# Kernel tuning notes

Measured on AMD Instinct MI355X. Metric: run time of the kernel, lower is better.

## Reference

```python
import jax, jax.numpy as jnp
import numpy as np
import math

N_HEADS = 16
D_EMB = 1024
D_HEAD = D_EMB // N_HEADS


def setup_inputs() -> dict:
    key = jax.random.key(0)
    ks = jax.random.split(key, 5)
    scale_in = 1.0 / math.sqrt(D_EMB)
    x = jax.random.normal(ks[0], (2, 2048, D_EMB), dtype=jnp.float32)
    w_in = jax.random.uniform(ks[1], (3 * D_EMB, D_EMB), dtype=jnp.float32, minval=-scale_in, maxval=scale_in)
    b_in = jax.random.uniform(ks[2], (3 * D_EMB,), dtype=jnp.float32, minval=-scale_in, maxval=scale_in)
    w_out = jax.random.uniform(ks[3], (D_EMB, D_EMB), dtype=jnp.float32, minval=-scale_in, maxval=scale_in)
    b_out = jax.random.uniform(ks[4], (D_EMB,), dtype=jnp.float32, minval=-scale_in, maxval=scale_in)
    return {"x": x, "w_in": w_in, "b_in": b_in, "w_out": w_out, "b_out": b_out, "apply_mask": 1}


def reference(x, w_in, b_in, w_out, b_out, apply_mask):
    B, S, D = x.shape
    # fused QKV projection: torch Linear uses y = x @ W^T + b
    qkv = jnp.einsum('bsd,ed->bse', x, w_in) + b_in  # [B,S,3D]
    q, k, v = jnp.split(qkv, 3, axis=-1)
    # [B,H,S,Dh]
    q = q.reshape(B, S, N_HEADS, D_HEAD).transpose(0, 2, 1, 3)
    k = k.reshape(B, S, N_HEADS, D_HEAD).transpose(0, 2, 1, 3)
    v = v.reshape(B, S, N_HEADS, D_HEAD).transpose(0, 2, 1, 3)
    w = jnp.einsum('bhqd,bhkd->bhqk', q, k)  # [B,H,S,S]
    if apply_mask:
        causal = jnp.triu(jnp.ones((S, S), dtype=bool), k=1)
        w = jnp.where(causal, -jnp.inf, w)
    w = w / jnp.sqrt(jnp.float32(D_HEAD)).astype(w.dtype)
    w = jax.nn.softmax(w, axis=-1)
    score = jnp.einsum('bhqk,bhkd->bhqd', w, v)  # [B,H,S,Dh]
    score = score.transpose(0, 2, 1, 3).reshape(B, S, D)
    return jnp.einsum('bsd,ed->bse', score, w_out) + b_out
```

## Files before the change

### kernel.cpp

```cpp
#include <hip/hip_runtime.h>
#include <stdint.h>

#define DEMB 1024
#define NHEAD 16
#define DHEAD 64
#define SEQ 2048
#define MROWS 4096

typedef __bf16 bf16x8 __attribute__((ext_vector_type(8)));
typedef float f32x4 __attribute__((ext_vector_type(4)));
typedef unsigned short u16;

#define LOG2E 1.44269504088896340736f

__device__ __forceinline__ u16 f2b(float f) {
  return __builtin_bit_cast(u16, (__bf16)f);
}
__device__ __forceinline__ uint32_t pk2(float a, float b) {
  return (uint32_t)f2b(a) | ((uint32_t)f2b(b) << 16);
}

__device__ __forceinline__ f32x4 mfma16(bf16x8 a, bf16x8 b, f32x4 c) {
  return __builtin_amdgcn_mfma_f32_16x16x32_bf16(a, b, c, 0, 0, 0);
}

__device__ __forceinline__ void gload_lds16(const void* g, void* l) {
  __builtin_amdgcn_global_load_lds(
      (__attribute__((address_space(1))) unsigned int*)(g),
      (__attribute__((address_space(3))) unsigned int*)(l), 16, 0, 0);
}

__device__ __forceinline__ void tile_barrier() {
  __builtin_amdgcn_sched_barrier(0);
  asm volatile("s_waitcnt vmcnt(0) lgkmcnt(0)" ::: "memory");
  __builtin_amdgcn_s_barrier();
  __builtin_amdgcn_sched_barrier(0);
}

__global__ void cvt3_f32_bf16(const float* __restrict__ a, int na,
                              const float* __restrict__ b, int nb,
                              const float* __restrict__ c, int nc,
                              u16* __restrict__ da, u16* __restrict__ db,
                              u16* __restrict__ dc) {
  const int total = (na + nb + nc) >> 2;
  const int stride = gridDim.x * blockDim.x;
  for (int t = blockIdx.x * blockDim.x + threadIdx.x; t < total; t += stride) {
    int i = t << 2;
    const float* s;
    u16* d;
    if (i < na) {
      s = a + i; d = da + i;
    } else if (i < na + nb) {
      s = b + (i - na); d = db + (i - na);
    } else {
      s = c + (i - na - nb); d = dc + (i - na - nb);
    }
    float4 f = *(const float4*)s;
    ushort4 o;
    o.x = f2b(f.x); o.y = f2b(f.y); o.z = f2b(f.z); o.w = f2b(f.w);
    *(ushort4*)d = o;
  }
}

template <int EPI>
__global__ __launch_bounds__(256, 2) void gemm_nt(
    const u16* __restrict__ A, const u16* __restrict__ Bw,
    const float* __restrict__ bias, int K, int N,
    u16* __restrict__ q_out, u16* __restrict__ k_out, u16* __restrict__ v_out,
    float* __restrict__ f_out) {
  __shared__ __align__(16) u16 As[128 * 64];
  __shared__ __align__(16) u16 Bs[128 * 64];
  const int tid = threadIdx.x;
  const int w = tid >> 6;
  const int lane = tid & 63;
  const int wm = w >> 1, wn = w & 1;
  const int m0 = blockIdx.y * 128, n0 = blockIdx.x * 128;
  const int l16 = lane & 15, lg = lane >> 4;
  const int st_row = lane >> 3, st_slot = lane & 7;

  f32x4 acc[4][4] = {};

  for (int k0 = 0; k0 < K; k0 += 64) {
#pragma unroll
    for (int i = 0; i < 4; ++i) {
      const int chunk = (w << 2) | i;
      const int row = (chunk << 3) | st_row;
      const int scol = (st_slot ^ (row & 7)) << 3;
      gload_lds16(A + (size_t)(m0 + row) * K + k0 + scol, (char*)As + (chunk << 10));
      gload_lds16(Bw + (size_t)(n0 + row) * K + k0 + scol, (char*)Bs + (chunk << 10));
    }
    __syncthreads();
#pragma unroll
    for (int ks = 0; ks < 2; ++ks) {
      bf16x8 af[4], bfr[4];
#pragma unroll
      for (int mi = 0; mi < 4; ++mi) {
        const int row = wm * 64 + mi * 16 + l16;
        const int cb = ((ks << 6) | (lg << 4)) ^ ((row & 7) << 4);
        af[mi] = *(const bf16x8*)((const char*)As + row * 128 + cb);
      }
#pragma unroll
      for (int ni = 0; ni < 4; ++ni) {
        const int row = wn * 64 + ni * 16 + l16;
        const int cb = ((ks << 6) | (lg << 4)) ^ ((row & 7) << 4);
        bfr[ni] = *(const bf16x8*)((const char*)Bs + row * 128 + cb);
      }
#pragma unroll
      for (int mi = 0; mi < 4; ++mi)
#pragma unroll
        for (int ni = 0; ni < 4; ++ni)
          acc[mi][ni] = mfma16(af[mi], bfr[ni], acc[mi][ni]);
    }
    __syncthreads();
  }

#pragma unroll
  for (int ni = 0; ni < 4; ++ni) {
    const int n = n0 + wn * 64 + ni * 16 + l16;
    const float bv = bias[n];
    if (EPI == 0) {
      const int part = n >> 10;
      const int hh = (n >> 6) & 15;
      const int dh = n & 63;
      if (part == 2) {
#pragma unroll
        for (int mi = 0; mi < 4; ++mi) {
          const int mbase = m0 + wm * 64 + mi * 16 + (lg << 2);
          const int bq = mbase >> 11, s0 = mbase & 2047;
          ushort4 o;
          o.x = f2b(acc[mi][ni][0] + bv);
          o.y = f2b(acc[mi][ni][1] + bv);
          o.z = f2b(acc[mi][ni][2] + bv);
          o.w = f2b(acc[mi][ni][3] + bv);
          *(ushort4*)(v_out + ((size_t)(((bq << 4) | hh) * 64 + dh)) * SEQ + s0) = o;
        }
      } else {
        const float scl = (part == 0) ? (0.125f * LOG2E) : 1.0f;
        u16* dst = (part == 0) ? q_out : k_out;
#pragma unroll
        for (int mi = 0; mi < 4; ++mi) {
#pragma unroll
          for (int i = 0; i < 4; ++i) {
            const int m = m0 + wm * 64 + mi * 16 + (lg << 2) + i;
            const int bq = m >> 11, s = m & 2047;
            dst[((size_t)((bq << 4) | hh) * SEQ + s) * DHEAD + dh] = f2b((acc[mi][ni][i] + bv) * scl);
          }
        }
      }
    } else {
#pragma unroll
      for (int mi = 0; mi < 4; ++mi)
#pragma unroll
        for (int i = 0; i < 4; ++i) {
          const int m = m0 + wm * 64 + mi * 16 + (lg << 2) + i;
          f_out[(size_t)m * N + n] = acc[mi][ni][i] + bv;
        }
    }
  }
}

__device__ __forceinline__ int swz4(int r) { return (r ^ (r >> 3)) & 15; }

__device__ __forceinline__ void stage_k(const u16* __restrict__ Kb, size_t base,
                                        int jt, u16* Ks, int w, int lane) {
#pragma unroll
  for (int i = 0; i < 4; ++i) {
    const int g = (w << 2) | i;
    const int row = (g << 2) | (lane >> 4);
    const int shat = (lane & 15) ^ swz4(row);
    const int kv = (row << 1) | (shat >> 3);
    const int del = (shat & 7) << 3;
    gload_lds16(Kb + base + (size_t)(jt * 128 + kv) * DHEAD + del,
                (char*)Ks + (g << 10));
  }
}

__device__ __forceinline__ void stage_v(const u16* __restrict__ VTg, size_t base,
                                        int jt, u16* Vs, int w, int lane) {
#pragma unroll
  for (int i = 0; i < 4; ++i) {
    const int g = (w << 2) | i;
    const int row = (g << 2) | (lane >> 4);
    const int shat = (lane & 15) ^ swz4(row);
    gload_lds16(VTg + base + (size_t)row * SEQ + jt * 128 + (shat << 3),
                (char*)Vs + (g << 10));
  }
}

__global__ __launch_bounds__(256, 2) void attn_fwd(
    const u16* __restrict__ Qb, const u16* __restrict__ Kb,
    const u16* __restrict__ VTg, u16* __restrict__ Ob,
    const int* __restrict__ amask) {
  __shared__ __align__(16) u16 Ks[2][64 * 128];
  __shared__ __align__(16) u16 Vt[2][64 * 128];
  __shared__ __align__(16) uint32_t Ps[4][1024];
  const int tid = threadIdx.x;
  const int w = tid >> 6, lane = tid & 63;
  const int l16 = lane & 15, lg = lane >> 4;

  const int id = blockIdx.x;
  const int xcd = id & 7;
  const int r = id >> 3;
  const int bh = (xcd << 2) | (r & 3);
  const int p = r >> 2;
  const int qiA = 31 - p, qiB = p;

  const size_t base = (size_t)bh * (SEQ * DHEAD);
  const bool causal = (amask[0] != 0);
  const int ntA = causal ? ((qiA >> 1) + 1) : (SEQ / 128);
  const int ntB = causal ? ((qiB >> 1) + 1) : (SEQ / 128);
  const int nt = ntA + ntB;
  const int b = bh >> 4, h = bh & 15;

  int qseg0 = qiA * 64;

  bf16x8 qf[2];
  {
    const u16* qp = Qb + base + (size_t)(qseg0 + (w << 4) + l16) * DHEAD + (lg << 3);
    qf[0] = *(const bf16x8*)qp;
    qf[1] = *(const bf16x8*)(qp + 32);
  }

  float mrow = -1e30f, lrow = 0.f;
  f32x4 oacc[4] = {};

  const int key = (l16 & 7) << 2;
  char* prow = (char*)(&Ps[w][0]) + l16 * 256;

  stage_k(Kb, base, 0, Ks[0], w, lane);
  stage_v(VTg, base, 0, Vt[0], w, lane);
  tile_barrier();

  int cur = 0;
  for (int t = 0; t < nt; ++t) {
    const int j = (t >= ntA) ? (t - ntA) : t;
    const u16* Kcur = Ks[cur];
    const u16* Vcur = Vt[cur];
    const bool pre = (t + 1 < nt);
    if (pre) {
      const int jn = (t + 1 >= ntA) ? (t + 1 - ntA) : (t + 1);
      stage_k(Kb, base, jn, Ks[cur ^ 1], w, lane);
      stage_v(VTg, base, jn, Vt[cur ^ 1], w, lane);
    }

    f32x4 sv[8];
    __builtin_amdgcn_s_setprio(1);
#pragma unroll
    for (int nf = 0; nf < 8; ++nf) {
      const int row2 = (nf << 3) | (l16 >> 1);
      const int sz = swz4(row2);
      const int s0 = ((l16 & 1) << 3) | lg;
      bf16x8 kf0 = *(const bf16x8*)((const char*)Kcur + row2 * 256 + ((s0 ^ sz) << 4));
      bf16x8 kf1 = *(const bf16x8*)((const char*)Kcur + row2 * 256 + (((s0 | 4) ^ sz) << 4));
      f32x4 s = {};
      s = mfma16(kf0, qf[0], s);
      s = mfma16(kf1, qf[1], s);
      sv[nf] = s;
    }
    __builtin_amdgcn_s_setprio(0);

    const bool segEnd = (t == ntA - 1) || (t == nt - 1);
    if (causal && segEnd) {
      const int q = qseg0 + (w << 4) + l16;
#pragma unroll
      for (int nf = 0; nf < 8; ++nf)
#pragma unroll
        for (int i = 0; i < 4; ++i) {
          const int kv = j * 128 + (nf << 4) + (lg << 2) + i;
          if (kv > q) sv[nf][i] = -1e30f;
        }
    }

    float tmax;
    {
      f32x4 m01, m23, m45, m67, ma, mb, mt;
#pragma unroll
      for (int i = 0; i < 4; ++i) {
        m01[i] = fmaxf(sv[0][i], sv[1][i]);
        m23[i] = fmaxf(sv[2][i], sv[3][i]);
        m45[i] = fmaxf(sv[4][i], sv[5][i]);
        m67[i] = fmaxf(sv[6][i], sv[7][i]);
        ma[i] = fmaxf(m01[i], m23[i]);
        mb[i] = fmaxf(m45[i], m67[i]);
        mt[i] = fmaxf(ma[i], mb[i]);
      }
      tmax = fmaxf(fmaxf(mt[0], mt[1]), fmaxf(mt[2], mt[3]));
      tmax = fmaxf(tmax, __shfl_xor(tmax, 16));
      tmax = fmaxf(tmax, __shfl_xor(tmax, 32));
    }

    if (__any(tmax > mrow + 8.0f)) {
      const float mnew = fmaxf(mrow, tmax);
      const float corr = __builtin_amdgcn_exp2f(mrow - mnew);
      mrow = mnew;
      lrow *= corr;
#pragma unroll
      for (int df = 0; df < 4; ++df)
#pragma unroll
        for (int i = 0; i < 4; ++i) oacc[df][i] *= corr;
    }

    float ps0 = 0.f, ps1 = 0.f;
#pragma unroll
    for (int nf = 0; nf < 8; ++nf) {
      const float p0 = __builtin_amdgcn_exp2f(sv[nf][0] - mrow);
      const float p1 = __builtin_amdgcn_exp2f(sv[nf][1] - mrow);
      const float p2 = __builtin_amdgcn_exp2f(sv[nf][2] - mrow);
      const float p3 = __builtin_amdgcn_exp2f(sv[nf][3] - mrow);
      ps0 += p0 + p1;
      ps1 += p2 + p3;
      uint2 pkv;
      pkv.x = pk2(p0, p1);
      pkv.y = pk2(p2, p3);
      const int word = ((nf << 3) | (lg << 1)) ^ key;
      *(uint2*)(prow + word * 4) = pkv;
    }
    float psum = ps0 + ps1;
    psum += __shfl_xor(psum, 16);
    psum += __shfl_xor(psum, 32);
    lrow += psum;

    bf16x8 pa[4];
#pragma unroll
    for (int s = 0; s < 4; ++s)
      pa[s] = *(const bf16x8*)(prow + ((((s << 4) | (lg << 2)) ^ key) << 2));

    __builtin_amdgcn_s_setprio(1);
#pragma unroll
    for (int df = 0; df < 4; ++df) {
      const int row = (df << 4) + l16;
      const int sz = swz4(row) << 4;
#pragma unroll
      for (int s = 0; s < 4; ++s) {
        bf16x8 vf = *(const bf16x8*)((const char*)Vcur + row * 256 + (((s << 6) | (lg << 4)) ^ sz));
        oacc[df] = mfma16(vf, pa[s], oacc[df]);
      }
    }
    __builtin_amdgcn_s_setprio(0);

    if (segEnd) {
      const float inv = 1.0f / lrow;
      const int s = qseg0 + (w << 4) + l16;
      u16* orow = Ob + (size_t)(b * SEQ + s) * DEMB + h * DHEAD;
#pragma unroll
      for (int df = 0; df < 4; ++df) {
        ushort4 o;
        o.x = f2b(oacc[df][0] * inv);
        o.y = f2b(oacc[df][1] * inv);
        o.z = f2b(oacc[df][2] * inv);
        o.w = f2b(oacc[df][3] * inv);
        *(ushort4*)(orow + (df << 4) + (lg << 2)) = o;
      }
      if (t != nt - 1) {
        qseg0 = qiB * 64;
        mrow = -1e30f;
        lrow = 0.f;
#pragma unroll
        for (int df = 0; df < 4; ++df)
#pragma unroll
          for (int i = 0; i < 4; ++i) oacc[df][i] = 0.f;
        const u16* qp = Qb + base + (size_t)(qseg0 + (w << 4) + l16) * DHEAD + (lg << 3);
        qf[0] = *(const bf16x8*)qp;
        qf[1] = *(const bf16x8*)(qp + 32);
      }
    }

    if (pre) tile_barrier();
    cur ^= 1;
  }
}

extern "C" void kernel_launch(void* const* d_in, const int* in_sizes, int n_in,
                              void* d_out, int out_size, void* d_ws, size_t ws_size,
                              hipStream_t stream) {
  const float* x = (const float*)d_in[0];
  const float* w_in = (const float*)d_in[1];
  const float* b_in = (const float*)d_in[2];
  const float* w_out = (const float*)d_in[3];
  const float* b_out = (const float*)d_in[4];
  const int* amask = (const int*)d_in[5];
  float* out = (float*)d_out;

  u16* xb = (u16*)d_ws;
  u16* wib = xb + (size_t)MROWS * DEMB;
  u16* wob = wib + (size_t)3 * DEMB * DEMB;
  u16* Qb = wob + (size_t)DEMB * DEMB;
  u16* Kb = Qb + (size_t)MROWS * DEMB;
  u16* Vtg = Kb + (size_t)MROWS * DEMB;
  u16* Ab = xb;

  cvt3_f32_bf16<<<2048, 256, 0, stream>>>(x, MROWS * DEMB, w_in, 3 * DEMB * DEMB,
                                          w_out, DEMB * DEMB, xb, wib, wob);

  gemm_nt<0><<<dim3(24, 32), 256, 0, stream>>>(xb, wib, b_in, DEMB, 3 * DEMB,
                                               Qb, Kb, Vtg, nullptr);
  attn_fwd<<<512, 256, 0, stream>>>(Qb, Kb, Vtg, Ab, amask);
  gemm_nt<1><<<dim3(8, 32), 256, 0, stream>>>(Ab, wob, b_out, DEMB, DEMB,
                                              nullptr, nullptr, nullptr, out);
}
```

Measured before the change: 102.2 us.

## Use 8-wave attention blocks over 128-row query tiles without segment pairing

The attention kernel now launches 512-thread blocks in which each block owns one 128-row query tile, with its eight waves sharing the staged K/V tiles. This replaces the earlier 4-wave blocks that each processed a paired long and short 64-row segment. The K/V staging work is split across the eight waves. The P scratch buffer is halved per wave and filled in two phases, separated by a scheduling barrier. The aim is more K/V reuse per LDS stage and simpler control flow, but causal work per block becomes uneven (only ordered largest-first), and the launch bound of 4 blocks per CU may force register pressure or spills even though LDS limits residency to fewer blocks.

```diff
diff --git a/kernel.cpp b/kernel.cpp
--- a/kernel.cpp
+++ b/kernel.cpp
@@ -164,8 +164,8 @@
 __device__ __forceinline__ void stage_k(const u16* __restrict__ Kb, size_t base,
                                         int jt, u16* Ks, int w, int lane) {
 #pragma unroll
-  for (int i = 0; i < 4; ++i) {
-    const int g = (w << 2) | i;
+  for (int i = 0; i < 2; ++i) {
+    const int g = (w << 1) | i;
     const int row = (g << 2) | (lane >> 4);
     const int shat = (lane & 15) ^ swz4(row);
     const int kv = (row << 1) | (shat >> 3);
@@ -178,8 +178,8 @@
 __device__ __forceinline__ void stage_v(const u16* __restrict__ VTg, size_t base,
                                         int jt, u16* Vs, int w, int lane) {
 #pragma unroll
-  for (int i = 0; i < 4; ++i) {
-    const int g = (w << 2) | i;
+  for (int i = 0; i < 2; ++i) {
+    const int g = (w << 1) | i;
     const int row = (g << 2) | (lane >> 4);
     const int shat = (lane & 15) ^ swz4(row);
     gload_lds16(VTg + base + (size_t)row * SEQ + jt * 128 + (shat << 3),
@@ -187,13 +187,13 @@
   }
 }
 
-__global__ __launch_bounds__(256, 2) void attn_fwd(
+__global__ __launch_bounds__(512, 4) void attn_fwd(
     const u16* __restrict__ Qb, const u16* __restrict__ Kb,
     const u16* __restrict__ VTg, u16* __restrict__ Ob,
     const int* __restrict__ amask) {
   __shared__ __align__(16) u16 Ks[2][64 * 128];
   __shared__ __align__(16) u16 Vt[2][64 * 128];
-  __shared__ __align__(16) uint32_t Ps[4][1024];
+  __shared__ __align__(16) uint32_t Ps[8][512];
   const int tid = threadIdx.x;
   const int w = tid >> 6, lane = tid & 63;
   const int l16 = lane & 15, lg = lane >> 4;
@@ -202,21 +202,17 @@
   const int xcd = id & 7;
   const int r = id >> 3;
   const int bh = (xcd << 2) | (r & 3);
-  const int p = r >> 2;
-  const int qiA = 31 - p, qiB = p;
+  const int qi = 15 - (r >> 2);
 
   const size_t base = (size_t)bh * (SEQ * DHEAD);
   const bool causal = (amask[0] != 0);
-  const int ntA = causal ? ((qiA >> 1) + 1) : (SEQ / 128);
-  const int ntB = causal ? ((qiB >> 1) + 1) : (SEQ / 128);
-  const int nt = ntA + ntB;
+  const int nt = causal ? (qi + 1) : (SEQ / 128);
   const int b = bh >> 4, h = bh & 15;
-
-  int qseg0 = qiA * 64;
+  const int qrow = qi * 128 + (w << 4) + l16;
 
   bf16x8 qf[2];
   {
-    const u16* qp = Qb + base + (size_t)(qseg0 + (w << 4) + l16) * DHEAD + (lg << 3);
+    const u16* qp = Qb + base + (size_t)qrow * DHEAD + (lg << 3);
     qf[0] = *(const bf16x8*)qp;
     qf[1] = *(const bf16x8*)(qp + 32);
   }
@@ -225,7 +221,7 @@
   f32x4 oacc[4] = {};
 
   const int key = (l16 & 7) << 2;
-  char* prow = (char*)(&Ps[w][0]) + l16 * 256;
+  char* prow = (char*)(&Ps[w][0]) + l16 * 128;
 
   stage_k(Kb, base, 0, Ks[0], w, lane);
   stage_v(VTg, base, 0, Vt[0], w, lane);
@@ -233,14 +229,12 @@
 
   int cur = 0;
   for (int t = 0; t < nt; ++t) {
-    const int j = (t >= ntA) ? (t - ntA) : t;
     const u16* Kcur = Ks[cur];
     const u16* Vcur = Vt[cur];
     const bool pre = (t + 1 < nt);
     if (pre) {
-      const int jn = (t + 1 >= ntA) ? (t + 1 - ntA) : (t + 1);
-      stage_k(Kb, base, jn, Ks[cur ^ 1], w, lane);
-      stage_v(VTg, base, jn, Vt[cur ^ 1], w, lane);
+      stage_k(Kb, base, t + 1, Ks[cur ^ 1], w, lane);
+      stage_v(VTg, base, t + 1, Vt[cur ^ 1], w, lane);
     }
 
     f32x4 sv[8];
@@ -259,15 +253,13 @@
     }
     __builtin_amdgcn_s_setprio(0);
 
-    const bool segEnd = (t == ntA - 1) || (t == nt - 1);
-    if (causal && segEnd) {
-      const int q = qseg0 + (w << 4) + l16;
+    if (causal && (t == nt - 1)) {
 #pragma unroll
       for (int nf = 0; nf < 8; ++nf)
 #pragma unroll
         for (int i = 0; i < 4; ++i) {
-          const int kv = j * 128 + (nf << 4) + (lg << 2) + i;
-          if (kv > q) sv[nf][i] = -1e30f;
+          const int kv = t * 128 + (nf << 4) + (lg << 2) + i;
+          if (kv > qrow) sv[nf][i] = -1e30f;
         }
     }
 
@@ -300,73 +292,71 @@
         for (int i = 0; i < 4; ++i) oacc[df][i] *= corr;
     }
 
-    float ps0 = 0.f, ps1 = 0.f;
+    float psum = 0.f;
+    uint2 pkv[8];
 #pragma unroll
     for (int nf = 0; nf < 8; ++nf) {
       const float p0 = __builtin_amdgcn_exp2f(sv[nf][0] - mrow);
       const float p1 = __builtin_amdgcn_exp2f(sv[nf][1] - mrow);
       const float p2 = __builtin_amdgcn_exp2f(sv[nf][2] - mrow);
       const float p3 = __builtin_amdgcn_exp2f(sv[nf][3] - mrow);
-      ps0 += p0 + p1;
-      ps1 += p2 + p3;
-      uint2 pkv;
-      pkv.x = pk2(p0, p1);
-      pkv.y = pk2(p2, p3);
-      const int word = ((nf << 3) | (lg << 1)) ^ key;
-      *(uint2*)(prow + word * 4) = pkv;
-    }
-    float psum = ps0 + ps1;
+      psum += (p0 + p1) + (p2 + p3);
+      pkv[nf].x = pk2(p0, p1);
+      pkv[nf].y = pk2(p2, p3);
+    }
     psum += __shfl_xor(psum, 16);
     psum += __shfl_xor(psum, 32);
     lrow += psum;
 
-    bf16x8 pa[4];
-#pragma unroll
-    for (int s = 0; s < 4; ++s)
-      pa[s] = *(const bf16x8*)(prow + ((((s << 4) | (lg << 2)) ^ key) << 2));
+    bf16x8 pa0, pa1, pa2, pa3;
+#pragma unroll
+    for (int nf = 0; nf < 4; ++nf) {
+      const int word = ((nf << 3) | (lg << 1)) ^ key;
+      *(uint2*)(prow + word * 4) = pkv[nf];
+    }
+    pa0 = *(const bf16x8*)(prow + ((((lg << 2)) ^ key) << 2));
+    pa1 = *(const bf16x8*)(prow + (((16 | (lg << 2)) ^ key) << 2));
+    __builtin_amdgcn_sched_barrier(0);
+#pragma unroll
+    for (int nf = 4; nf < 8; ++nf) {
+      const int word = (((nf - 4) << 3) | (lg << 1)) ^ key;
+      *(uint2*)(prow + word * 4) = pkv[nf];
+    }
+    pa2 = *(const bf16x8*)(prow + ((((lg << 2)) ^ key) << 2));
+    pa3 = *(const bf16x8*)(prow + (((16 | (lg << 2)) ^ key) << 2));
 
     __builtin_amdgcn_s_setprio(1);
 #pragma unroll
     for (int df = 0; df < 4; ++df) {
       const int row = (df << 4) + l16;
       const int sz = swz4(row) << 4;
-#pragma unroll
-      for (int s = 0; s < 4; ++s) {
-        bf16x8 vf = *(const bf16x8*)((const char*)Vcur + row * 256 + (((s << 6) | (lg << 4)) ^ sz));
-        oacc[df] = mfma16(vf, pa[s], oacc[df]);
-      }
+      bf16x8 vf0 = *(const bf16x8*)((const char*)Vcur + row * 256 + (((0 << 6) | (lg << 4)) ^ sz));
+      bf16x8 vf1 = *(const bf16x8*)((const char*)Vcur + row * 256 + (((1 << 6) | (lg << 4)) ^ sz));
+      bf16x8 vf2 = *(const bf16x8*)((const char*)Vcur + row * 256 + (((2 << 6) | (lg << 4)) ^ sz));
+      bf16x8 vf3 = *(const bf16x8*)((const char*)Vcur + row * 256 + (((3 << 6) | (lg << 4)) ^ sz));
+      oacc[df] = mfma16(vf0, pa0, oacc[df]);
+      oacc[df] = mfma16(vf1, pa1, oacc[df]);
+      oacc[df] = mfma16(vf2, pa2, oacc[df]);
+      oacc[df] = mfma16(vf3, pa3, oacc[df]);
     }
     __builtin_amdgcn_s_setprio(0);
-
-    if (segEnd) {
-      const float inv = 1.0f / lrow;
-      const int s = qseg0 + (w << 4) + l16;
-      u16* orow = Ob + (size_t)(b * SEQ + s) * DEMB + h * DHEAD;
-#pragma unroll
-      for (int df = 0; df < 4; ++df) {
-        ushort4 o;
-        o.x = f2b(oacc[df][0] * inv);
-        o.y = f2b(oacc[df][1] * inv);
-        o.z = f2b(oacc[df][2] * inv);
-        o.w = f2b(oacc[df][3] * inv);
-        *(ushort4*)(orow + (df << 4) + (lg << 2)) = o;
-      }
-      if (t != nt - 1) {
-        qseg0 = qiB * 64;
-        mrow = -1e30f;
-        lrow = 0.f;
-#pragma unroll
-        for (int df = 0; df < 4; ++df)
-#pragma unroll
-          for (int i = 0; i < 4; ++i) oacc[df][i] = 0.f;
-        const u16* qp = Qb + base + (size_t)(qseg0 + (w << 4) + l16) * DHEAD + (lg << 3);
-        qf[0] = *(const bf16x8*)qp;
-        qf[1] = *(const bf16x8*)(qp + 32);
-      }
-    }
 
     if (pre) tile_barrier();
     cur ^= 1;
+  }
+
+  {
+    const float inv = 1.0f / lrow;
+    u16* orow = Ob + (size_t)(b * SEQ + qrow) * DEMB + h * DHEAD;
+#pragma unroll
+    for (int df = 0; df < 4; ++df) {
+      ushort4 o;
+      o.x = f2b(oacc[df][0] * inv);
+      o.y = f2b(oacc[df][1] * inv);
+      o.z = f2b(oacc[df][2] * inv);
+      o.w = f2b(oacc[df][3] * inv);
+      *(ushort4*)(orow + (df << 4) + (lg << 2)) = o;
+    }
   }
 }
 
@@ -394,7 +384,7 @@
 
   gemm_nt<0><<<dim3(24, 32), 256, 0, stream>>>(xb, wib, b_in, DEMB, 3 * DEMB,
                                                Qb, Kb, Vtg, nullptr);
-  attn_fwd<<<512, 256, 0, stream>>>(Qb, Kb, Vtg, Ab, amask);
+  attn_fwd<<<512, 512, 0, stream>>>(Qb, Kb, Vtg, Ab, amask);
   gemm_nt<1><<<dim3(8, 32), 256, 0, stream>>>(Ab, wob, b_out, DEMB, DEMB,
                                               nullptr, nullptr, nullptr, out);
 }
```

Result: slower. 111.0 us (+8.6%).
